# Kernel tuning notes

Hardware: AMD Instinct MI355X
Metric: run time of the kernel (lower is better)

Reference implementation:

```python
import jax, jax.numpy as jnp
import numpy as np

IN_FEATURES = 2048
OUT_FEATURES = 2048
BATCH = 4096


def setup_inputs() -> dict:
    key = jax.random.key(0)
    kx, kw, kb, kp = jax.random.split(key, 4)
    x = jax.random.normal(kx, (BATCH, IN_FEATURES), dtype=jnp.float32)
    weight = jax.random.normal(kw, (OUT_FEATURES, IN_FEATURES), dtype=jnp.float32)
    bias = jax.random.normal(kb, (OUT_FEATURES,), dtype=jnp.float32)
    # torch uses torch.randperm(in_features) at forward time; we fix a permutation here
    indices = jax.random.permutation(kp, IN_FEATURES).astype(jnp.int64)
    return {"x": x, "weight": weight, "bias": bias, "indices": indices}


def reference(x, weight, bias, indices):
    # Original: (x[:, None, :] * weight)[:, :, indices].sum(dim=2) + bias
    # Summing the permuted reduction axis == contracting the permuted operands;
    # we gather both x and weight along the permutation then do a real GEMM,
    # avoiding the huge [B, out, in] intermediate while keeping identical math.
    xp = x[:, indices]            # [B, in]
    wp = weight[:, indices]       # [out, in]
    return jnp.einsum('bi,oi->bo', xp, wp) + bias[None, :]
```

## Files before the change

### kernel.cpp

```cpp
#include <hip/hip_runtime.h>
#include <hip/hip_bf16.h>

#define M_DIM 4096
#define N_DIM 2048
#define K_DIM 2048

#define BM 128
#define BN 128
#define BK 32
#define NT (K_DIM / BK)
#define BUF_EL 8192

typedef __bf16 bf16x8 __attribute__((ext_vector_type(8)));
typedef float f32x4 __attribute__((ext_vector_type(4)));
typedef int   i32x4 __attribute__((ext_vector_type(4)));
typedef unsigned short u16x8 __attribute__((ext_vector_type(8)));

__device__ __forceinline__ unsigned short f32_to_bf16_rne(float f) {
  unsigned int u = __float_as_uint(f);
  u += 0x7fffu + ((u >> 16) & 1u);
  return (unsigned short)(u >> 16);
}

__global__ __launch_bounds__(256) void cvt_both(
    const float* __restrict__ x, const float* __restrict__ w,
    unsigned short* __restrict__ out, int xn8, int totn8) {
  int i = blockIdx.x * 256 + threadIdx.x;
  if (i >= totn8) return;
  const float* src = (i < xn8) ? (x + (size_t)i * 8)
                               : (w + (size_t)(i - xn8) * 8);
  f32x4 a = reinterpret_cast<const f32x4*>(src)[0];
  f32x4 b = reinterpret_cast<const f32x4*>(src)[1];
  u16x8 o;
  o[0] = f32_to_bf16_rne(a[0]); o[1] = f32_to_bf16_rne(a[1]);
  o[2] = f32_to_bf16_rne(a[2]); o[3] = f32_to_bf16_rne(a[3]);
  o[4] = f32_to_bf16_rne(b[0]); o[5] = f32_to_bf16_rne(b[1]);
  o[6] = f32_to_bf16_rne(b[2]); o[7] = f32_to_bf16_rne(b[3]);
  reinterpret_cast<u16x8*>(out)[i] = o;
}

__device__ __forceinline__ void gload_lds16(const unsigned short* g, unsigned short* l) {
  __builtin_amdgcn_global_load_lds(
      (const __attribute__((address_space(1))) unsigned int*)g,
      (__attribute__((address_space(3))) unsigned int*)l, 16, 0, 0);
}

#define VMWAIT_(n) asm volatile("s_waitcnt vmcnt(" #n ")" ::: "memory")
#define VMWAIT(n) VMWAIT_(n)
#define LGKM0() do { \
    asm volatile("s_waitcnt lgkmcnt(0)" ::: "memory"); \
    __builtin_amdgcn_sched_barrier(0); \
  } while (0)
#define SBAR() __builtin_amdgcn_s_barrier()
#define SCHED() __builtin_amdgcn_sched_barrier(0)

#define DSREAD(dst, addr, OFS) \
  asm volatile("ds_read_b128 %0, %1 offset:" OFS : "=v"(dst) : "v"(addr))

#define BCAST(v) __builtin_bit_cast(bf16x8, v)

__global__ __launch_bounds__(256, 2) void gemm_asm(
    const unsigned short* __restrict__ A,
    const unsigned short* __restrict__ B,
    const float* __restrict__ bias,
    float* __restrict__ C) {
  __shared__ unsigned short L[3 * BUF_EL];

  const int tid  = threadIdx.x;
  const int lane = tid & 63;
  const int wave = tid >> 6;
  const int wr   = wave >> 1;
  const int wc   = wave & 1;

  const int orig = blockIdx.x;
  const int xcd  = orig & 7;
  const int idx  = orig >> 3;
  const int bm   = (xcd & 3) * 8 + (idx & 7);
  const int bn   = (xcd >> 2) * 8 + (idx >> 3);

  const int lid  = tid >> 3;
  const int uu   = (tid & 7) ^ (lid & 7);
  const int grow = 2 * lid + (uu >> 2);
  const int kc   = (uu & 3) * 8;
  const unsigned short* Ag[2];
  const unsigned short* Bg[2];
#pragma unroll
  for (int j = 0; j < 2; ++j) {
    Ag[j] = A + (size_t)(bm * BM + j * 64 + grow) * K_DIM + kc;
    Bg[j] = B + (size_t)(bn * BN + j * 64 + grow) * K_DIM + kc;
  }

#define STAGE(bufLit, k0) do { \
    unsigned short* _da = &L[(bufLit) * BUF_EL + tid * 8]; \
    unsigned short* _db = &L[(bufLit) * BUF_EL + 4096 + tid * 8]; \
    gload_lds16(Ag[0] + (k0), _da); \
    gload_lds16(Ag[1] + (k0), _da + 2048); \
    gload_lds16(Bg[0] + (k0), _db); \
    gload_lds16(Bg[1] + (k0), _db + 2048); \
  } while (0)

  const int fr = lane & 15;
  const int qq = lane >> 4;
  unsigned adrA[4], adrB[4];
  {
    const unsigned base = (unsigned)(uintptr_t)(&L[0]);
#pragma unroll
    for (int mi = 0; mi < 4; ++mi) {
      const int R = wr * 64 + mi * 16 + fr;
      const int e = (R >> 1) * 64 + ((((R & 1) * 4 + qq) ^ ((R >> 1) & 7)) * 8);
      adrA[mi] = base + e * 2;
    }
#pragma unroll
    for (int ni = 0; ni < 4; ++ni) {
      const int R = wc * 64 + ni * 16 + fr;
      const int e = (R >> 1) * 64 + ((((R & 1) * 4 + qq) ^ ((R >> 1) & 7)) * 8);
      adrB[ni] = base + 8192 + e * 2;
    }
  }

  const f32x4 z = {0.f, 0.f, 0.f, 0.f};
  f32x4 acc[4][4];
#pragma unroll
  for (int i = 0; i < 4; ++i)
#pragma unroll
    for (int j = 0; j < 4; ++j) acc[i][j] = z;

  i32x4 Xa0, Xa1, Xa2, Xa3, Xb0, Xb1, Xb2, Xb3;
  i32x4 Ya0, Ya1, Ya2, Ya3, Yb0, Yb1, Yb2, Yb3;

#define READ_X(OFS) do { \
    DSREAD(Xb0, adrB[0], OFS); DSREAD(Xb1, adrB[1], OFS); \
    DSREAD(Xb2, adrB[2], OFS); DSREAD(Xb3, adrB[3], OFS); \
    DSREAD(Xa0, adrA[0], OFS); DSREAD(Xa1, adrA[1], OFS); \
    DSREAD(Xa2, adrA[2], OFS); DSREAD(Xa3, adrA[3], OFS); \
  } while (0)
#define READ_Y(OFS) do { \
    DSREAD(Yb0, adrB[0], OFS); DSREAD(Yb1, adrB[1], OFS); \
    DSREAD(Yb2, adrB[2], OFS); DSREAD(Yb3, adrB[3], OFS); \
    DSREAD(Ya0, adrA[0], OFS); DSREAD(Ya1, adrA[1], OFS); \
    DSREAD(Ya2, adrA[2], OFS); DSREAD(Ya3, adrA[3], OFS); \
  } while (0)

#define MFMA_ROW(a_, b0_, b1_, b2_, b3_, mi) do { \
    acc[mi][0] = __builtin_amdgcn_mfma_f32_16x16x32_bf16(BCAST(a_), BCAST(b0_), acc[mi][0], 0, 0, 0); \
    acc[mi][1] = __builtin_amdgcn_mfma_f32_16x16x32_bf16(BCAST(a_), BCAST(b1_), acc[mi][1], 0, 0, 0); \
    acc[mi][2] = __builtin_amdgcn_mfma_f32_16x16x32_bf16(BCAST(a_), BCAST(b2_), acc[mi][2], 0, 0, 0); \
    acc[mi][3] = __builtin_amdgcn_mfma_f32_16x16x32_bf16(BCAST(a_), BCAST(b3_), acc[mi][3], 0, 0, 0); \
  } while (0)

#define MFMA_X() do { \
    __builtin_amdgcn_s_setprio(1); \
    MFMA_ROW(Xa0, Xb0, Xb1, Xb2, Xb3, 0); \
    MFMA_ROW(Xa1, Xb0, Xb1, Xb2, Xb3, 1); \
    MFMA_ROW(Xa2, Xb0, Xb1, Xb2, Xb3, 2); \
    MFMA_ROW(Xa3, Xb0, Xb1, Xb2, Xb3, 3); \
    __builtin_amdgcn_s_setprio(0); \
  } while (0)
#define MFMA_Y() do { \
    __builtin_amdgcn_s_setprio(1); \
    MFMA_ROW(Ya0, Yb0, Yb1, Yb2, Yb3, 0); \
    MFMA_ROW(Ya1, Yb0, Yb1, Yb2, Yb3, 1); \
    MFMA_ROW(Ya2, Yb0, Yb1, Yb2, Yb3, 2); \
    MFMA_ROW(Ya3, Yb0, Yb1, Yb2, Yb3, 3); \
    __builtin_amdgcn_s_setprio(0); \
  } while (0)

#define TILE_X(stgB, OFSRD, k0) do { \
    STAGE(stgB, k0); VMWAIT(4); SBAR(); SCHED(); \
    READ_Y(OFSRD); SCHED(); \
    MFMA_X(); \
    LGKM0(); \
    SBAR(); \
  } while (0)
#define TILE_Y(stgB, OFSRD, k0) do { \
    STAGE(stgB, k0); VMWAIT(4); SBAR(); SCHED(); \
    READ_X(OFSRD); SCHED(); \
    MFMA_Y(); \
    LGKM0(); \
    SBAR(); \
  } while (0)

  STAGE(0, 0);
  STAGE(1, BK);
  VMWAIT(4);
  SBAR();
  SCHED();
  READ_X("0");
  LGKM0();

#pragma unroll 1
  for (int s = 0; s < 10; ++s) {
    const int kb = (6 * s + 2) * BK;
    TILE_X(2, "16384", kb);
    TILE_Y(0, "32768", kb + BK);
    TILE_X(1, "0",     kb + 2 * BK);
    TILE_Y(2, "16384", kb + 3 * BK);
    TILE_X(0, "32768", kb + 4 * BK);
    TILE_Y(1, "0",     kb + 5 * BK);
  }

  TILE_X(2, "16384", 62 * BK);
  TILE_Y(0, "32768", 63 * BK);
  VMWAIT(0);
  SBAR();
  SCHED();
  READ_Y("0");
  SCHED();
  MFMA_X();
  LGKM0();
  MFMA_Y();

  const int orow0 = bm * BM + wr * 64 + qq * 4;
  const int ocol0 = bn * BN + wc * 64 + fr;
#pragma unroll
  for (int ni = 0; ni < 4; ++ni) {
    const int col = ocol0 + ni * 16;
    const float bvv = bias[col];
#pragma unroll
    for (int mi = 0; mi < 4; ++mi) {
      const int row = orow0 + mi * 16;
#pragma unroll
      for (int r = 0; r < 4; ++r)
        C[(size_t)(row + r) * N_DIM + col] = acc[mi][ni][r] + bvv;
    }
  }
#undef TILE_X
#undef TILE_Y
#undef MFMA_X
#undef MFMA_Y
#undef MFMA_ROW
#undef READ_X
#undef READ_Y
#undef STAGE
}

__global__ __launch_bounds__(256) void gemm_f32_naive(
    const float* __restrict__ X, const float* __restrict__ W,
    const float* __restrict__ bias, float* __restrict__ C) {
  int o = blockIdx.x * 256 + threadIdx.x;
  if (o >= M_DIM * N_DIM) return;
  int m = o / N_DIM, n = o % N_DIM;
  const float* xr = X + (size_t)m * K_DIM;
  const float* wr = W + (size_t)n * K_DIM;
  float s = 0.f;
  for (int k = 0; k < K_DIM; ++k) s += xr[k] * wr[k];
  C[o] = s + bias[n];
}

extern "C" void kernel_launch(void* const* d_in, const int* in_sizes, int n_in,
                              void* d_out, int out_size, void* d_ws, size_t ws_size,
                              hipStream_t stream) {
  const float* x    = (const float*)d_in[0];
  const float* w    = (const float*)d_in[1];
  const float* bias = (const float*)d_in[2];
  float* out = (float*)d_out;

  const size_t x_elems = (size_t)M_DIM * K_DIM;
  const size_t w_elems = (size_t)N_DIM * K_DIM;
  const size_t need = (x_elems + w_elems) * sizeof(unsigned short);

  if (ws_size < need) {
    gemm_f32_naive<<<(M_DIM * N_DIM + 255) / 256, 256, 0, stream>>>(x, w, bias, out);
    return;
  }

  unsigned short* xb = (unsigned short*)d_ws;
  unsigned short* wb = xb + x_elems;

  const int xn8 = (int)(x_elems / 8);
  const int totn8 = (int)((x_elems + w_elems) / 8);
  cvt_both<<<(totn8 + 255) / 256, 256, 0, stream>>>(x, w, xb, xn8, totn8);

  gemm_asm<<<512, 256, 0, stream>>>(xb, wb, bias, out);
}
```

Measured before the change: 56.75 us.

## Use four LDS buffers with one barrier per K-tile and deferred staging

```diff
diff --git a/kernel.cpp b/kernel.cpp
--- a/kernel.cpp
+++ b/kernel.cpp
@@ -47,10 +47,7 @@
 
 #define VMWAIT_(n) asm volatile("s_waitcnt vmcnt(" #n ")" ::: "memory")
 #define VMWAIT(n) VMWAIT_(n)
-#define LGKM0() do { \
-    asm volatile("s_waitcnt lgkmcnt(0)" ::: "memory"); \
-    __builtin_amdgcn_sched_barrier(0); \
-  } while (0)
+#define LGKM_(n) asm volatile("s_waitcnt lgkmcnt(" #n ")" ::: "memory")
 #define SBAR() __builtin_amdgcn_s_barrier()
 #define SCHED() __builtin_amdgcn_sched_barrier(0)
 
@@ -59,12 +56,12 @@
 
 #define BCAST(v) __builtin_bit_cast(bf16x8, v)
 
-__global__ __launch_bounds__(256, 2) void gemm_asm(
+__global__ __launch_bounds__(256, 2) void gemm_1b(
     const unsigned short* __restrict__ A,
     const unsigned short* __restrict__ B,
     const float* __restrict__ bias,
     float* __restrict__ C) {
-  __shared__ unsigned short L[3 * BUF_EL];
+  __shared__ unsigned short L[4 * BUF_EL];
 
   const int tid  = threadIdx.x;
   const int lane = tid & 63;
@@ -165,49 +162,48 @@
     __builtin_amdgcn_s_setprio(0); \
   } while (0)
 
-#define TILE_X(stgB, OFSRD, k0) do { \
-    STAGE(stgB, k0); VMWAIT(4); SBAR(); SCHED(); \
-    READ_Y(OFSRD); SCHED(); \
+#define TILE_X(RDOFS, stgB, k0) do { \
+    VMWAIT(4); SBAR(); SCHED(); \
+    READ_Y(RDOFS); \
+    LGKM_(8); SCHED(); \
     MFMA_X(); \
-    LGKM0(); \
-    SBAR(); \
-  } while (0)
-#define TILE_Y(stgB, OFSRD, k0) do { \
-    STAGE(stgB, k0); VMWAIT(4); SBAR(); SCHED(); \
-    READ_X(OFSRD); SCHED(); \
+    STAGE(stgB, k0); \
+  } while (0)
+#define TILE_Y(RDOFS, stgB, k0) do { \
+    VMWAIT(4); SBAR(); SCHED(); \
+    READ_X(RDOFS); \
+    LGKM_(8); SCHED(); \
     MFMA_Y(); \
-    LGKM0(); \
-    SBAR(); \
+    STAGE(stgB, k0); \
   } while (0)
 
   STAGE(0, 0);
   STAGE(1, BK);
-  VMWAIT(4);
+  STAGE(2, 2 * BK);
+  VMWAIT(8);
   SBAR();
   SCHED();
   READ_X("0");
-  LGKM0();
 
 #pragma unroll 1
-  for (int s = 0; s < 10; ++s) {
-    const int kb = (6 * s + 2) * BK;
-    TILE_X(2, "16384", kb);
-    TILE_Y(0, "32768", kb + BK);
-    TILE_X(1, "0",     kb + 2 * BK);
-    TILE_Y(2, "16384", kb + 3 * BK);
-    TILE_X(0, "32768", kb + 4 * BK);
-    TILE_Y(1, "0",     kb + 5 * BK);
-  }
-
-  TILE_X(2, "16384", 62 * BK);
-  TILE_Y(0, "32768", 63 * BK);
-  VMWAIT(0);
-  SBAR();
-  SCHED();
-  READ_Y("0");
-  SCHED();
+  for (int s = 0; s < 15; ++s) {
+    const int kb = (4 * s + 3) * BK;
+    TILE_X("16384", 3, kb);
+    TILE_Y("32768", 0, kb + BK);
+    TILE_X("49152", 1, kb + 2 * BK);
+    TILE_Y("0",     2, kb + 3 * BK);
+  }
+
+  TILE_X("16384", 3, 63 * BK);
+  VMWAIT(4); SBAR(); SCHED();
+  READ_X("32768");
+  LGKM_(8); SCHED();
+  MFMA_Y();
+  VMWAIT(0); SBAR(); SCHED();
+  READ_Y("49152");
+  LGKM_(8); SCHED();
   MFMA_X();
-  LGKM0();
+  LGKM_(0); SCHED();
   MFMA_Y();
 
   const int orow0 = bm * BM + wr * 64 + qq * 4;
@@ -271,5 +267,5 @@
   const int totn8 = (int)((x_elems + w_elems) / 8);
   cvt_both<<<(totn8 + 255) / 256, 256, 0, stream>>>(x, w, xb, xn8, totn8);
 
-  gemm_asm<<<512, 256, 0, stream>>>(xb, wb, bias, out);
-}
+  gemm_1b<<<512, 256, 0, stream>>>(xb, wb, bias, out);
+}
```

Result: no change. 56.73 us (-0.0%).
